# Kernel tuning notes

Measured on AMD Instinct MI355X. Metric: run time of the kernel, lower is better.

Reference implementation:

```python
import jax, jax.numpy as jnp
import numpy as np

T = 2048      # tokens
H = 1024      # hidden_size
HQ = 16       # num query heads
HK = 4        # num kv heads
D = 64        # head_dim
E = 8         # num experts
K = 2         # top_k
I = 2048      # expert intermediate size
EPS = 1e-5
THETA = 10000.0


def setup_inputs() -> dict:
    key = jax.random.key(0)
    ks = jax.random.split(key, 8)
    s = 0.02
    return {
        "hidden_states": jax.random.normal(ks[0], (T, H), jnp.float32),
        "positions": jnp.arange(T, dtype=jnp.int32),
        "qkv_w": jax.random.normal(ks[1], ((HQ + 2 * HK) * D, H), jnp.float32) * s,
        "o_w": jax.random.normal(ks[2], (H, HQ * D), jnp.float32) * s,
        "norm_in_w": jnp.ones((H,), jnp.float32),
        "norm_post_w": jnp.ones((H,), jnp.float32),
        "norm_next_w": jnp.ones((H,), jnp.float32),
        "gate_w": jax.random.normal(ks[3], (E, H), jnp.float32) * s,
        "w1": jax.random.normal(ks[4], (E, I, H), jnp.float32) * s,
        "w3": jax.random.normal(ks[5], (E, I, H), jnp.float32) * s,
        "w2": jax.random.normal(ks[6], (E, H, I), jnp.float32) * s,
    }


def rmsnorm(x, w):
    var = jnp.mean(x * x, axis=-1, keepdims=True)
    return x * jax.lax.rsqrt(var + EPS) * w


def rope_neox(x, positions):
    # x: [T, nH, D]; rotate-half (neox) style
    half = D // 2
    inv_freq = 1.0 / (THETA ** (jnp.arange(0, half, dtype=jnp.float32) * 2.0 / D))
    ang = positions.astype(jnp.float32)[:, None] * inv_freq[None, :]      # [T, D/2]
    cos = jnp.cos(ang)[:, None, :]
    sin = jnp.sin(ang)[:, None, :]
    x1, x2 = x[..., :half], x[..., half:]
    return jnp.concatenate([x1 * cos - x2 * sin, x2 * cos + x1 * sin], axis=-1)


def reference(hidden_states, positions, qkv_w, o_w, norm_in_w, norm_post_w,
              norm_next_w, gate_w, w1, w3, w2):
    x = hidden_states                               # [T, H]
    residual = x
    h = rmsnorm(x, norm_in_w)                       # input_layernorm

    # ---- attention (GQA, causal, neox RoPE) ----
    qkv = h @ qkv_w.T                               # [T, (HQ+2HK)*D]
    q, k, v = jnp.split(qkv, [HQ * D, (HQ + HK) * D], axis=-1)
    q = rope_neox(q.reshape(T, HQ, D), positions)
    k = rope_neox(k.reshape(T, HK, D), positions)
    v = v.reshape(T, HK, D)
    rep = HQ // HK
    k = jnp.repeat(k, rep, axis=1)                  # [T, HQ, D]
    v = jnp.repeat(v, rep, axis=1)
    scale = D ** -0.5
    scores = jnp.einsum('qhd,khd->hqk', q, k) * scale   # [HQ, T, T]
    mask = jnp.tril(jnp.ones((T, T), dtype=bool))
    scores = jnp.where(mask[None], scores, -jnp.inf)
    probs = jax.nn.softmax(scores, axis=-1)
    attn = jnp.einsum('hqk,khd->qhd', probs, v).reshape(T, HQ * D)
    attn_out = attn @ o_w.T                         # [T, H]

    # fused allreduce(identity, world=1) + residual add + post_attention RMSNorm
    residual = residual + attn_out
    h = rmsnorm(residual, norm_post_w)

    # ---- MoE: gate, top-2, renormalize, SiLU-gated experts ----
    logits = h @ gate_w.T                           # [T, E]
    route = jax.nn.softmax(logits, axis=-1)
    topw, topi = jax.lax.top_k(route, K)            # [T, K]
    topw = topw / jnp.sum(topw, axis=-1, keepdims=True)   # renormalize
    # dense combine weights [T, E] (zero for unselected experts)
    wdense = jnp.sum(jax.nn.one_hot(topi, E, dtype=h.dtype) * topw[..., None], axis=1)
    h1 = jnp.einsum('td,eid->tei', h, w1)           # [T, E, I]
    h3 = jnp.einsum('td,eid->tei', h, w3)
    gated = jax.nn.silu(h1) * h3
    moe_out = jnp.einsum('tei,edi,te->td', gated, w2, wdense)   # [T, H]

    # fused allreduce(identity) + residual add + next layer norm
    residual = residual + moe_out
    h = rmsnorm(residual, norm_next_w)
    return h
```

## Files before the change

kernel.cpp:

```cpp
#include <hip/hip_runtime.h>
#include <hip/hip_bf16.h>
#include <math.h>

#define T_ 2048
#define H_ 1024
#define HQ_ 16
#define HK_ 4
#define D_ 64
#define NE_ 8
#define II_ 2048

typedef __attribute__((ext_vector_type(8))) short bf16x8;
typedef __attribute__((ext_vector_type(8))) unsigned short u16x8;
typedef __attribute__((ext_vector_type(4))) float f32x4;

__device__ __forceinline__ unsigned short f2bf(float f) {
  unsigned int u = __float_as_uint(f);
  return (unsigned short)((u + 0x7fffu + ((u >> 16) & 1u)) >> 16);
}
__device__ __forceinline__ float bf2f(unsigned short h) {
  return __uint_as_float((unsigned int)h << 16);
}

__global__ __launch_bounds__(256) void k_rmsnorm(const float* __restrict__ x, const float* __restrict__ w,
                                                 float* __restrict__ outf, unsigned short* __restrict__ outb) {
  int row = blockIdx.x;
  int tid = threadIdx.x;
  float4 v = ((const float4*)(x + (size_t)row * H_))[tid];
  float ss = v.x * v.x + v.y * v.y + v.z * v.z + v.w * v.w;
#pragma unroll
  for (int off = 32; off; off >>= 1) ss += __shfl_xor(ss, off, 64);
  __shared__ float red[4];
  int lane = tid & 63, wid = tid >> 6;
  if (lane == 0) red[wid] = ss;
  __syncthreads();
  float tot = red[0] + red[1] + red[2] + red[3];
  float inv = rsqrtf(tot * (1.0f / H_) + 1e-5f);
  float4 wv = ((const float4*)w)[tid];
  float4 o;
  o.x = v.x * inv * wv.x; o.y = v.y * inv * wv.y; o.z = v.z * inv * wv.z; o.w = v.w * inv * wv.w;
  ((float4*)(outf + (size_t)row * H_))[tid] = o;
  if (outb) {
    ushort4 b; b.x = f2bf(o.x); b.y = f2bf(o.y); b.z = f2bf(o.z); b.w = f2bf(o.w);
    ((ushort4*)(outb + (size_t)row * H_))[tid] = b;
  }
}

__global__ __launch_bounds__(256) void k_rmsnorm_split(const float* __restrict__ x, const float* __restrict__ w,
                                                       unsigned short* __restrict__ Aq) {
  int row = blockIdx.x;
  int tid = threadIdx.x;
  float4 v = ((const float4*)(x + (size_t)row * H_))[tid];
  float ss = v.x * v.x + v.y * v.y + v.z * v.z + v.w * v.w;
#pragma unroll
  for (int off = 32; off; off >>= 1) ss += __shfl_xor(ss, off, 64);
  __shared__ float red[4];
  int lane = tid & 63, wid = tid >> 6;
  if (lane == 0) red[wid] = ss;
  __syncthreads();
  float tot = red[0] + red[1] + red[2] + red[3];
  float inv = rsqrtf(tot * (1.0f / H_) + 1e-5f);
  float4 wv = ((const float4*)w)[tid];
  float4 o;
  o.x = v.x * inv * wv.x; o.y = v.y * inv * wv.y; o.z = v.z * inv * wv.z; o.w = v.w * inv * wv.w;
  ushort4 hi, lo;
  hi.x = f2bf(o.x); hi.y = f2bf(o.y); hi.z = f2bf(o.z); hi.w = f2bf(o.w);
  lo.x = f2bf(o.x - bf2f(hi.x)); lo.y = f2bf(o.y - bf2f(hi.y));
  lo.z = f2bf(o.z - bf2f(hi.z)); lo.w = f2bf(o.w - bf2f(hi.w));
  size_t base = (size_t)row * (3 * H_) + tid * 4;
  *(ushort4*)(Aq + base) = hi;
  *(ushort4*)(Aq + base + H_) = hi;
  *(ushort4*)(Aq + base + 2 * H_) = lo;
}

__global__ __launch_bounds__(256) void k_wsplit(const float* __restrict__ in, unsigned short* __restrict__ out,
                                                int K, int n8total) {
  int stride = gridDim.x * 256;
  int kc8 = K >> 3;
  for (int i = blockIdx.x * 256 + threadIdx.x; i < n8total; i += stride) {
    int n = i / kc8, kc = (i - n * kc8) * 8;
    const float4* p = (const float4*)(in + (size_t)n * K + kc);
    float4 a = p[0], b = p[1];
    u16x8 hi, lo;
    hi[0] = f2bf(a.x); hi[1] = f2bf(a.y); hi[2] = f2bf(a.z); hi[3] = f2bf(a.w);
    hi[4] = f2bf(b.x); hi[5] = f2bf(b.y); hi[6] = f2bf(b.z); hi[7] = f2bf(b.w);
    lo[0] = f2bf(a.x - bf2f(hi[0])); lo[1] = f2bf(a.y - bf2f(hi[1]));
    lo[2] = f2bf(a.z - bf2f(hi[2])); lo[3] = f2bf(a.w - bf2f(hi[3]));
    lo[4] = f2bf(b.x - bf2f(hi[4])); lo[5] = f2bf(b.y - bf2f(hi[5]));
    lo[6] = f2bf(b.z - bf2f(hi[6])); lo[7] = f2bf(b.w - bf2f(hi[7]));
    size_t ob = (size_t)n * 3 * K + kc;
    *(u16x8*)(out + ob) = hi;
    *(u16x8*)(out + ob + K) = lo;
    *(u16x8*)(out + ob + 2 * K) = hi;
  }
}

template <int ADD>
__global__ __launch_bounds__(256) void k_hgemm(const unsigned short* __restrict__ A, const unsigned short* __restrict__ B,
                                               float* __restrict__ C, const float* __restrict__ addsrc,
                                               int N, int K3) {
  int m0 = blockIdx.y * 128, n0 = blockIdx.x * 64;
  __shared__ unsigned short As[2][128 * 72];
  __shared__ unsigned short Bs[2][64 * 72];
  int tid = threadIdx.x, lane = tid & 63, wid = tid >> 6;
  int wr = wid >> 1, wc = wid & 1;
  int l15 = lane & 15, lg = lane >> 4;
  int arow = tid >> 3, akg = (tid & 7) * 8;

  size_t aoff[4];
#pragma unroll
  for (int i = 0; i < 4; i++) aoff[i] = (size_t)(m0 + arow + 32 * i) * K3 + akg;
  size_t boff[2];
#pragma unroll
  for (int j = 0; j < 2; j++) boff[j] = (size_t)(n0 + arow + 32 * j) * K3 + akg;

  f32x4 acc[4][2];
  f32x4 z = {0.f, 0.f, 0.f, 0.f};
#pragma unroll
  for (int a = 0; a < 4; a++)
#pragma unroll
    for (int b = 0; b < 2; b++) acc[a][b] = z;

  uint4 pa[4], pb[2];
#pragma unroll
  for (int i = 0; i < 4; i++) pa[i] = *(const uint4*)(A + aoff[i]);
#pragma unroll
  for (int j = 0; j < 2; j++) pb[j] = *(const uint4*)(B + boff[j]);
#pragma unroll
  for (int i = 0; i < 4; i++) *(uint4*)&As[0][(arow + 32 * i) * 72 + akg] = pa[i];
#pragma unroll
  for (int j = 0; j < 2; j++) *(uint4*)&Bs[0][(arow + 32 * j) * 72 + akg] = pb[j];
  __syncthreads();
  int cur = 0;
  int nt = K3 / 64;
  for (int t = 0; t < nt; ++t) {
    if (t < nt - 1) {
      int kn = (t + 1) * 64;
#pragma unroll
      for (int i = 0; i < 4; i++) pa[i] = *(const uint4*)(A + aoff[i] + kn);
#pragma unroll
      for (int j = 0; j < 2; j++) pb[j] = *(const uint4*)(B + boff[j] + kn);
    }
#pragma unroll
    for (int kk = 0; kk < 2; kk++) {
      bf16x8 af[4], bw[2];
#pragma unroll
      for (int fa = 0; fa < 4; fa++)
        af[fa] = *(const bf16x8*)&As[cur][(wr * 64 + fa * 16 + l15) * 72 + kk * 32 + lg * 8];
#pragma unroll
      for (int fb = 0; fb < 2; fb++)
        bw[fb] = *(const bf16x8*)&Bs[cur][(wc * 32 + fb * 16 + l15) * 72 + kk * 32 + lg * 8];
#pragma unroll
      for (int fa = 0; fa < 4; fa++)
#pragma unroll
        for (int fb = 0; fb < 2; fb++)
          acc[fa][fb] = __builtin_amdgcn_mfma_f32_16x16x32_bf16(af[fa], bw[fb], acc[fa][fb], 0, 0, 0);
    }
    if (t < nt - 1) {
#pragma unroll
      for (int i = 0; i < 4; i++) *(uint4*)&As[cur ^ 1][(arow + 32 * i) * 72 + akg] = pa[i];
#pragma unroll
      for (int j = 0; j < 2; j++) *(uint4*)&Bs[cur ^ 1][(arow + 32 * j) * 72 + akg] = pb[j];
    }
    __syncthreads();
    cur ^= 1;
  }
#pragma unroll
  for (int fa = 0; fa < 4; fa++)
#pragma unroll
    for (int r = 0; r < 4; r++) {
      int row = m0 + wr * 64 + fa * 16 + lg * 4 + r;
#pragma unroll
      for (int fb = 0; fb < 2; fb++) {
        int col = n0 + wc * 32 + fb * 16 + l15;
        float v = acc[fa][fb][r];
        if (ADD) v += addsrc[(size_t)row * N + col];
        C[(size_t)row * N + col] = v;
      }
    }
}

__global__ __launch_bounds__(256) void k_rope_table(const int* __restrict__ pos, float* __restrict__ ct,
                                                    float* __restrict__ st) {
  int idx = blockIdx.x * 256 + threadIdx.x;
  int t = idx >> 5, i = idx & 31;
  float p = (float)pow(10000.0, (double)i / 32.0);
  float freq = 1.0f / p;
  float ang = (float)pos[t] * freq;
  ct[idx] = cosf(ang);
  st[idx] = sinf(ang);
}

__global__ __launch_bounds__(256) void k_rope_prep(const float* __restrict__ qkv, const float* __restrict__ ct,
                                                   const float* __restrict__ st, unsigned short* __restrict__ Qhi,
                                                   unsigned short* __restrict__ Qlo, unsigned short* __restrict__ Khi,
                                                   unsigned short* __restrict__ Klo) {
  int t = blockIdx.x, tid = threadIdx.x;
  const float* row = qkv + (size_t)t * 1536;
#pragma unroll 2
  for (int it = tid; it < 512; it += 256) {
    int h = it >> 5, i = it & 31;
    float c = ct[t * 32 + i], s = st[t * 32 + i];
    float x1 = row[h * 64 + i], x2 = row[h * 64 + i + 32];
    float a = (x1 * c - x2 * s) * 0.125f;
    float b = (x2 * c + x1 * s) * 0.125f;
    size_t base = ((size_t)h * T_ + t) * 64 + i;
    unsigned short ah = f2bf(a), bh = f2bf(b);
    Qhi[base] = ah; Qhi[base + 32] = bh;
    Qlo[base] = f2bf(a - bf2f(ah));
    Qlo[base + 32] = f2bf(b - bf2f(bh));
  }
  if (tid < 128) {
    int h = tid >> 5, i = tid & 31;
    float c = ct[t * 32 + i], s = st[t * 32 + i];
    float x1 = row[1024 + h * 64 + i], x2 = row[1024 + h * 64 + i + 32];
    float a = x1 * c - x2 * s;
    float b = x2 * c + x1 * s;
    size_t base = ((size_t)h * T_ + t) * 64 + i;
    unsigned short ah = f2bf(a), bh = f2bf(b);
    Khi[base] = ah; Khi[base + 32] = bh;
    Klo[base] = f2bf(a - bf2f(ah));
    Klo[base + 32] = f2bf(b - bf2f(bh));
  }
}

__global__ __launch_bounds__(256) void k_vtrans(const float* __restrict__ qkv, unsigned short* __restrict__ Vthi,
                                                unsigned short* __restrict__ Vtlo) {
  int t0 = blockIdx.x * 64, h = blockIdx.y;
  __shared__ float tile[64][65];
  int tid = threadIdx.x;
  int c = tid & 63, w = tid >> 6;
  for (int r = w; r < 64; r += 4)
    tile[r][c] = qkv[(size_t)(t0 + r) * 1536 + 1280 + h * 64 + c];
  __syncthreads();
  for (int d = w; d < 64; d += 4) {
    float v = tile[c][d];
    unsigned short hi = f2bf(v);
    size_t idx = ((size_t)h * 64 + d) * T_ + t0 + c;
    Vthi[idx] = hi;
    Vtlo[idx] = f2bf(v - bf2f(hi));
  }
}

__global__ __launch_bounds__(256) void k_attn_mfma(const unsigned short* __restrict__ Qhi,
                                                   const unsigned short* __restrict__ Qlo,
                                                   const unsigned short* __restrict__ Khi,
                                                   const unsigned short* __restrict__ Klo,
                                                   const unsigned short* __restrict__ Vthi,
                                                   const unsigned short* __restrict__ Vtlo,
                                                   unsigned short* __restrict__ Ao) {
  int bid = blockIdx.x;
  int kk = bid >> 4;
  int head = bid & 15;
  int qidx = (kk < 16) ? (31 - kk) : (kk - 16);
  int qb = qidx * 64;
  int kvh = head >> 2;
  int tid = threadIdx.x, lane = tid & 63, w = tid >> 6;
  int l15 = lane & 15, lg = lane >> 4;

  __shared__ unsigned short KsH[64 * 72], KsL[64 * 72];
  __shared__ unsigned short VsH[64 * 72], VsL[64 * 72];
  __shared__ unsigned short PsH[64 * 72], PsL[64 * 72];

  bf16x8 qh[2], ql[2];
  {
    size_t qbase = ((size_t)head * T_ + qb + w * 16 + l15) * 64 + lg * 8;
    qh[0] = *(const bf16x8*)(Qhi + qbase);
    qh[1] = *(const bf16x8*)(Qhi + qbase + 32);
    ql[0] = *(const bf16x8*)(Qlo + qbase);
    ql[1] = *(const bf16x8*)(Qlo + qbase + 32);
  }
  f32x4 z = {0.f, 0.f, 0.f, 0.f};
  f32x4 Oa[4];
  float mrow[4], lrow[4];
#pragma unroll
  for (int r = 0; r < 4; r++) { mrow[r] = -1e30f; lrow[r] = 0.f; }
#pragma unroll
  for (int dg = 0; dg < 4; dg++) Oa[dg] = z;

  for (int jb = 0; jb <= qb; jb += 64) {
    __syncthreads();
    for (int c = tid; c < 512; c += 256) {
      int r = c >> 3, g = (c & 7) * 8;
      size_t kgl = ((size_t)kvh * T_ + jb + r) * 64 + g;
      size_t vgl = ((size_t)kvh * 64 + r) * T_ + jb + g;
      *(uint4*)&KsH[r * 72 + g] = *(const uint4*)(Khi + kgl);
      *(uint4*)&KsL[r * 72 + g] = *(const uint4*)(Klo + kgl);
      *(uint4*)&VsH[r * 72 + g] = *(const uint4*)(Vthi + vgl);
      *(uint4*)&VsL[r * 72 + g] = *(const uint4*)(Vtlo + vgl);
    }
    __syncthreads();

    f32x4 sc[4];
    sc[0] = z; sc[1] = z; sc[2] = z; sc[3] = z;
#pragma unroll
    for (int kg = 0; kg < 4; kg++) {
      int ba = (kg * 16 + l15) * 72 + lg * 8;
      bf16x8 bh0 = *(const bf16x8*)&KsH[ba];
      bf16x8 bh1 = *(const bf16x8*)&KsH[ba + 32];
      bf16x8 bl0 = *(const bf16x8*)&KsL[ba];
      bf16x8 bl1 = *(const bf16x8*)&KsL[ba + 32];
      sc[kg] = __builtin_amdgcn_mfma_f32_16x16x32_bf16(qh[0], bh0, sc[kg], 0, 0, 0);
      sc[kg] = __builtin_amdgcn_mfma_f32_16x16x32_bf16(qh[1], bh1, sc[kg], 0, 0, 0);
      sc[kg] = __builtin_amdgcn_mfma_f32_16x16x32_bf16(qh[0], bl0, sc[kg], 0, 0, 0);
      sc[kg] = __builtin_amdgcn_mfma_f32_16x16x32_bf16(qh[1], bl1, sc[kg], 0, 0, 0);
      sc[kg] = __builtin_amdgcn_mfma_f32_16x16x32_bf16(ql[0], bh0, sc[kg], 0, 0, 0);
      sc[kg] = __builtin_amdgcn_mfma_f32_16x16x32_bf16(ql[1], bh1, sc[kg], 0, 0, 0);
    }
    if (jb == qb) {
      int rb = w * 16 + lg * 4;
#pragma unroll
      for (int kg = 0; kg < 4; kg++) {
        int col = kg * 16 + l15;
#pragma unroll
        for (int r = 0; r < 4; r++)
          if (col > rb + r) sc[kg][r] = -1e30f;
      }
    }
#pragma unroll
    for (int r = 0; r < 4; r++) {
      float mt = fmaxf(fmaxf(sc[0][r], sc[1][r]), fmaxf(sc[2][r], sc[3][r]));
      mt = fmaxf(mt, __shfl_xor(mt, 1, 64));
      mt = fmaxf(mt, __shfl_xor(mt, 2, 64));
      mt = fmaxf(mt, __shfl_xor(mt, 4, 64));
      mt = fmaxf(mt, __shfl_xor(mt, 8, 64));
      float mnew = fmaxf(mrow[r], mt);
      float corr = __expf(mrow[r] - mnew);
      mrow[r] = mnew;
      float s = 0.f;
#pragma unroll
      for (int kg = 0; kg < 4; kg++) {
        float p = __expf(sc[kg][r] - mnew);
        sc[kg][r] = p;
        s += p;
      }
      s += __shfl_xor(s, 1, 64);
      s += __shfl_xor(s, 2, 64);
      s += __shfl_xor(s, 4, 64);
      s += __shfl_xor(s, 8, 64);
      lrow[r] = lrow[r] * corr + s;
#pragma unroll
      for (int dg = 0; dg < 4; dg++) Oa[dg][r] *= corr;
    }
    {
      int rb = w * 16 + lg * 4;
#pragma unroll
      for (int kg = 0; kg < 4; kg++) {
        int col = kg * 16 + l15;
#pragma unroll
        for (int r = 0; r < 4; r++) {
          float p = sc[kg][r];
          unsigned short ph = f2bf(p);
          PsH[(rb + r) * 72 + col] = ph;
          PsL[(rb + r) * 72 + col] = f2bf(p - bf2f(ph));
        }
      }
    }
    {
      int ab = (w * 16 + l15) * 72 + lg * 8;
      bf16x8 ph0 = *(const bf16x8*)&PsH[ab];
      bf16x8 ph1 = *(const bf16x8*)&PsH[ab + 32];
      bf16x8 pl0 = *(const bf16x8*)&PsL[ab];
      bf16x8 pl1 = *(const bf16x8*)&PsL[ab + 32];
#pragma unroll
      for (int dg = 0; dg < 4; dg++) {
        int vb = (dg * 16 + l15) * 72 + lg * 8;
        bf16x8 vh0 = *(const bf16x8*)&VsH[vb];
        bf16x8 vh1 = *(const bf16x8*)&VsH[vb + 32];
        bf16x8 vl0 = *(const bf16x8*)&VsL[vb];
        bf16x8 vl1 = *(const bf16x8*)&VsL[vb + 32];
        Oa[dg] = __builtin_amdgcn_mfma_f32_16x16x32_bf16(ph0, vh0, Oa[dg], 0, 0, 0);
        Oa[dg] = __builtin_amdgcn_mfma_f32_16x16x32_bf16(ph1, vh1, Oa[dg], 0, 0, 0);
        Oa[dg] = __builtin_amdgcn_mfma_f32_16x16x32_bf16(ph0, vl0, Oa[dg], 0, 0, 0);
        Oa[dg] = __builtin_amdgcn_mfma_f32_16x16x32_bf16(ph1, vl1, Oa[dg], 0, 0, 0);
        Oa[dg] = __builtin_amdgcn_mfma_f32_16x16x32_bf16(pl0, vh0, Oa[dg], 0, 0, 0);
        Oa[dg] = __builtin_amdgcn_mfma_f32_16x16x32_bf16(pl1, vh1, Oa[dg], 0, 0, 0);
      }
    }
  }
#pragma unroll
  for (int r = 0; r < 4; r++) {
    float inv = 1.0f / lrow[r];
    size_t rb2 = (size_t)(qb + w * 16 + lg * 4 + r) * 3072 + head * 64;
#pragma unroll
    for (int dg = 0; dg < 4; dg++) {
      float v = Oa[dg][r] * inv;
      unsigned short hi = f2bf(v);
      unsigned short lo = f2bf(v - bf2f(hi));
      Ao[rb2 + dg * 16 + l15] = hi;
      Ao[rb2 + 1024 + dg * 16 + l15] = hi;
      Ao[rb2 + 2048 + dg * 16 + l15] = lo;
    }
  }
}

__global__ __launch_bounds__(256) void k_router(const float* __restrict__ h2, const float* __restrict__ gw,
                                                int* __restrict__ topi, float* __restrict__ topw,
                                                int* __restrict__ counts) {
  int wid = threadIdx.x >> 6, lane = threadIdx.x & 63;
  int t = blockIdx.x * 4 + wid;
  const float* hr = h2 + (size_t)t * H_;
  float hv[16];
#pragma unroll
  for (int i = 0; i < 16; i++) hv[i] = hr[lane + 64 * i];
  float le[8];
#pragma unroll
  for (int e = 0; e < 8; e++) {
    const float* g = gw + (size_t)e * H_;
    float acc = 0.f;
#pragma unroll
    for (int i = 0; i < 16; i++) acc += hv[i] * g[lane + 64 * i];
#pragma unroll
    for (int off = 32; off; off >>= 1) acc += __shfl_xor(acc, off, 64);
    le[e] = acc;
  }
  if (lane == 0) {
    int i0 = 0;
#pragma unroll
    for (int e = 1; e < 8; e++)
      if (le[e] > le[i0]) i0 = e;
    int i1 = (i0 == 0) ? 1 : 0;
#pragma unroll
    for (int e = 0; e < 8; e++) {
      if (e == i0) continue;
      if (le[e] > le[i1]) i1 = e;
    }
    float w1r = expf(le[i1] - le[i0]);
    float denom = 1.0f + w1r;
    topi[t * 2 + 0] = i0;
    topi[t * 2 + 1] = i1;
    topw[t * 2 + 0] = 1.0f / denom;
    topw[t * 2 + 1] = w1r / denom;
    atomicAdd(&counts[i0], 1);
    atomicAdd(&counts[i1], 1);
  }
}

__global__ void k_scan(const int* __restrict__ counts, int* __restrict__ offsets) {
  if (threadIdx.x == 0 && blockIdx.x == 0) {
    int off = 0;
    for (int e = 0; e < NE_; e++) { offsets[e] = off; off += counts[e]; }
  }
}

__global__ __launch_bounds__(256) void k_build(const int* __restrict__ topi, const float* __restrict__ topw,
                                               const int* __restrict__ offsets, int* __restrict__ counts2,
                                               int* __restrict__ pairs_ts, float* __restrict__ pairs_w) {
  int t = blockIdx.x * 256 + threadIdx.x;
#pragma unroll
  for (int s = 0; s < 2; s++) {
    int e = topi[t * 2 + s];
    int slot = atomicAdd(&counts2[e], 1);
    int p = offsets[e] + slot;
    pairs_ts[p] = t * 2 + s;
    pairs_w[p] = topw[t * 2 + s];
  }
}

__global__ __launch_bounds__(256) void k_conv(const float* __restrict__ in, unsigned short* __restrict__ out, int n8) {
  int stride = gridDim.x * 256;
  for (int i = blockIdx.x * 256 + threadIdx.x; i < n8; i += stride) {
    const float4* p = (const float4*)in + (size_t)i * 2;
    float4 a = p[0], b = p[1];
    u16x8 t;
    t[0] = f2bf(a.x); t[1] = f2bf(a.y); t[2] = f2bf(a.z); t[3] = f2bf(a.w);
    t[4] = f2bf(b.x); t[5] = f2bf(b.y); t[6] = f2bf(b.z); t[7] = f2bf(b.w);
    *((u16x8*)out + i) = t;
  }
}

__global__ __launch_bounds__(256) void k_moe_up(const unsigned short* __restrict__ h2b, const unsigned short* __restrict__ W1b,
                                                const unsigned short* __restrict__ W3b, const int* __restrict__ pairs_ts,
                                                const int* __restrict__ offsets, const int* __restrict__ counts,
                                                unsigned short* __restrict__ G) {
  int e = blockIdx.z;
  int ne = counts[e];
  int row0 = blockIdx.y * 128;
  if (row0 >= ne) return;
  int col0 = blockIdx.x * 64;
  int pbase = offsets[e];
  __shared__ unsigned short As[2][128 * 72];
  __shared__ unsigned short B1s[2][64 * 72];
  __shared__ unsigned short B2s[2][64 * 72];
  int tid = threadIdx.x, lane = tid & 63, wid = tid >> 6;
  int wr = wid >> 1, wc = wid & 1;
  int l15 = lane & 15, lg = lane >> 4;
  int arow = tid >> 3, akg = (tid & 7) * 8;

  int aoff[4];
#pragma unroll
  for (int i = 0; i < 4; i++) {
    int grow = row0 + arow + 32 * i;
    int tok = (grow < ne) ? (pairs_ts[pbase + grow] >> 1) : 0;
    aoff[i] = tok * H_ + akg;
  }
  size_t bbase = ((size_t)e * II_ + col0 + arow) * H_ + akg;

  f32x4 acc1[4][2], acc2[4][2];
  f32x4 z = {0.f, 0.f, 0.f, 0.f};
#pragma unroll
  for (int a = 0; a < 4; a++)
#pragma unroll
    for (int b = 0; b < 2; b++) { acc1[a][b] = z; acc2[a][b] = z; }

  uint4 pa[4], pb1[2], pb2[2];
#pragma unroll
  for (int i = 0; i < 4; i++) pa[i] = *(const uint4*)(h2b + aoff[i]);
#pragma unroll
  for (int j = 0; j < 2; j++) {
    pb1[j] = *(const uint4*)(W1b + bbase + (size_t)j * 32 * H_);
    pb2[j] = *(const uint4*)(W3b + bbase + (size_t)j * 32 * H_);
  }
#pragma unroll
  for (int i = 0; i < 4; i++) *(uint4*)&As[0][(arow + 32 * i) * 72 + akg] = pa[i];
#pragma unroll
  for (int j = 0; j < 2; j++) {
    *(uint4*)&B1s[0][(arow + 32 * j) * 72 + akg] = pb1[j];
    *(uint4*)&B2s[0][(arow + 32 * j) * 72 + akg] = pb2[j];
  }
  __syncthreads();
  int cur = 0;
  for (int t = 0; t < H_ / 64; ++t) {
    if (t < H_ / 64 - 1) {
      int kn = (t + 1) * 64;
#pragma unroll
      for (int i = 0; i < 4; i++) pa[i] = *(const uint4*)(h2b + aoff[i] + kn);
#pragma unroll
      for (int j = 0; j < 2; j++) {
        pb1[j] = *(const uint4*)(W1b + bbase + (size_t)j * 32 * H_ + kn);
        pb2[j] = *(const uint4*)(W3b + bbase + (size_t)j * 32 * H_ + kn);
      }
    }
#pragma unroll
    for (int kk = 0; kk < 2; kk++) {
      bf16x8 af[4], b1f[2], b2f[2];
#pragma unroll
      for (int fa = 0; fa < 4; fa++)
        af[fa] = *(const bf16x8*)&As[cur][(wr * 64 + fa * 16 + l15) * 72 + kk * 32 + lg * 8];
#pragma unroll
      for (int fb = 0; fb < 2; fb++) {
        b1f[fb] = *(const bf16x8*)&B1s[cur][(wc * 32 + fb * 16 + l15) * 72 + kk * 32 + lg * 8];
        b2f[fb] = *(const bf16x8*)&B2s[cur][(wc * 32 + fb * 16 + l15) * 72 + kk * 32 + lg * 8];
      }
#pragma unroll
      for (int fa = 0; fa < 4; fa++)
#pragma unroll
        for (int fb = 0; fb < 2; fb++) {
          acc1[fa][fb] = __builtin_amdgcn_mfma_f32_16x16x32_bf16(af[fa], b1f[fb], acc1[fa][fb], 0, 0, 0);
          acc2[fa][fb] = __builtin_amdgcn_mfma_f32_16x16x32_bf16(af[fa], b2f[fb], acc2[fa][fb], 0, 0, 0);
        }
    }
    if (t < H_ / 64 - 1) {
#pragma unroll
      for (int i = 0; i < 4; i++) *(uint4*)&As[cur ^ 1][(arow + 32 * i) * 72 + akg] = pa[i];
#pragma unroll
      for (int j = 0; j < 2; j++) {
        *(uint4*)&B1s[cur ^ 1][(arow + 32 * j) * 72 + akg] = pb1[j];
        *(uint4*)&B2s[cur ^ 1][(arow + 32 * j) * 72 + akg] = pb2[j];
      }
    }
    __syncthreads();
    cur ^= 1;
  }
#pragma unroll
  for (int fa = 0; fa < 4; fa++)
#pragma unroll
    for (int r = 0; r < 4; r++) {
      int prow = row0 + wr * 64 + fa * 16 + lg * 4 + r;
      if (prow < ne) {
#pragma unroll
        for (int fb = 0; fb < 2; fb++) {
          int icol = col0 + wc * 32 + fb * 16 + l15;
          float h1 = acc1[fa][fb][r], h3 = acc2[fa][fb][r];
          float g = h1 / (1.0f + __expf(-h1)) * h3;
          G[(size_t)(pbase + prow) * II_ + icol] = f2bf(g);
        }
      }
    }
}

__global__ __launch_bounds__(256) void k_moe_down(const unsigned short* __restrict__ G, const unsigned short* __restrict__ W2b,
                                                  const int* __restrict__ pairs_ts, const float* __restrict__ pairs_w,
                                                  const int* __restrict__ offsets, const int* __restrict__ counts,
                                                  float* __restrict__ Pbuf) {
  int e = blockIdx.z;
  int ne = counts[e];
  int row0 = blockIdx.y * 128;
  if (row0 >= ne) return;
  int col0 = blockIdx.x * 64;
  int pbase = offsets[e];
  __shared__ unsigned short As[2][128 * 72];
  __shared__ unsigned short Bs[2][64 * 72];
  int tid = threadIdx.x, lane = tid & 63, wid = tid >> 6;
  int wr = wid >> 1, wc = wid & 1;
  int l15 = lane & 15, lg = lane >> 4;
  int arow = tid >> 3, akg = (tid & 7) * 8;

  int aoff[4];
#pragma unroll
  for (int i = 0; i < 4; i++) {
    int grow = row0 + arow + 32 * i;
    int p = pbase + ((grow < ne) ? grow : 0);
    aoff[i] = p * II_ + akg;
  }
  size_t bbase = ((size_t)e * H_ + col0 + arow) * II_ + akg;

  f32x4 acc[4][2];
  f32x4 z = {0.f, 0.f, 0.f, 0.f};
#pragma unroll
  for (int a = 0; a < 4; a++)
#pragma unroll
    for (int b = 0; b < 2; b++) acc[a][b] = z;

  uint4 pa[4], pb[2];
#pragma unroll
  for (int i = 0; i < 4; i++) pa[i] = *(const uint4*)(G + aoff[i]);
#pragma unroll
  for (int j = 0; j < 2; j++) pb[j] = *(const uint4*)(W2b + bbase + (size_t)j * 32 * II_);
#pragma unroll
  for (int i = 0; i < 4; i++) *(uint4*)&As[0][(arow + 32 * i) * 72 + akg] = pa[i];
#pragma unroll
  for (int j = 0; j < 2; j++) *(uint4*)&Bs[0][(arow + 32 * j) * 72 + akg] = pb[j];
  __syncthreads();
  int cur = 0;
  for (int t = 0; t < II_ / 64; ++t) {
    if (t < II_ / 64 - 1) {
      int kn = (t + 1) * 64;
#pragma unroll
      for (int i = 0; i < 4; i++) pa[i] = *(const uint4*)(G + aoff[i] + kn);
#pragma unroll
      for (int j = 0; j < 2; j++) pb[j] = *(const uint4*)(W2b + bbase + (size_t)j * 32 * II_ + kn);
    }
#pragma unroll
    for (int kk = 0; kk < 2; kk++) {
      bf16x8 af[4], bw[2];
#pragma unroll
      for (int fa = 0; fa < 4; fa++)
        af[fa] = *(const bf16x8*)&As[cur][(wr * 64 + fa * 16 + l15) * 72 + kk * 32 + lg * 8];
#pragma unroll
      for (int fb = 0; fb < 2; fb++)
        bw[fb] = *(const bf16x8*)&Bs[cur][(wc * 32 + fb * 16 + l15) * 72 + kk * 32 + lg * 8];
#pragma unroll
      for (int fa = 0; fa < 4; fa++)
#pragma unroll
        for (int fb = 0; fb < 2; fb++)
          acc[fa][fb] = __builtin_amdgcn_mfma_f32_16x16x32_bf16(af[fa], bw[fb], acc[fa][fb], 0, 0, 0);
    }
    if (t < II_ / 64 - 1) {
#pragma unroll
      for (int i = 0; i < 4; i++) *(uint4*)&As[cur ^ 1][(arow + 32 * i) * 72 + akg] = pa[i];
#pragma unroll
      for (int j = 0; j < 2; j++) *(uint4*)&Bs[cur ^ 1][(arow + 32 * j) * 72 + akg] = pb[j];
    }
    __syncthreads();
    cur ^= 1;
  }
#pragma unroll
  for (int fa = 0; fa < 4; fa++)
#pragma unroll
    for (int r = 0; r < 4; r++) {
      int prow = row0 + wr * 64 + fa * 16 + lg * 4 + r;
      if (prow < ne) {
        int p = pbase + prow;
        int ts = pairs_ts[p];
        float wgt = pairs_w[p];
#pragma unroll
        for (int fb = 0; fb < 2; fb++) {
          int col = col0 + wc * 32 + fb * 16 + l15;
          Pbuf[(size_t)ts * H_ + col] = wgt * acc[fa][fb][r];
        }
      }
    }
}

__global__ __launch_bounds__(256) void k_final(const float* __restrict__ resid, const float* __restrict__ Pbuf,
                                               const float* __restrict__ w, float* __restrict__ out) {
  int row = blockIdx.x;
  int tid = threadIdx.x;
  float4 a = ((const float4*)(resid + (size_t)row * H_))[tid];
  float4 p0 = ((const float4*)(Pbuf + (size_t)(2 * row) * H_))[tid];
  float4 p1 = ((const float4*)(Pbuf + (size_t)(2 * row + 1) * H_))[tid];
  float4 v;
  v.x = a.x + p0.x + p1.x; v.y = a.y + p0.y + p1.y; v.z = a.z + p0.z + p1.z; v.w = a.w + p0.w + p1.w;
  float ss = v.x * v.x + v.y * v.y + v.z * v.z + v.w * v.w;
#pragma unroll
  for (int off = 32; off; off >>= 1) ss += __shfl_xor(ss, off, 64);
  __shared__ float red[4];
  int lane = tid & 63, wid = tid >> 6;
  if (lane == 0) red[wid] = ss;
  __syncthreads();
  float tot = red[0] + red[1] + red[2] + red[3];
  float inv = rsqrtf(tot * (1.0f / H_) + 1e-5f);
  float4 wv = ((const float4*)w)[tid];
  float4 o;
  o.x = v.x * inv * wv.x; o.y = v.y * inv * wv.y; o.z = v.z * inv * wv.z; o.w = v.w * inv * wv.w;
  ((float4*)(out + (size_t)row * H_))[tid] = o;
}

extern "C" void kernel_launch(void* const* d_in, const int* in_sizes, int n_in,
                              void* d_out, int out_size, void* d_ws, size_t ws_size,
                              hipStream_t stream) {
  const float* x = (const float*)d_in[0];
  const int* pos = (const int*)d_in[1];
  const float* qkv_w = (const float*)d_in[2];
  const float* o_w = (const float*)d_in[3];
  const float* nin_w = (const float*)d_in[4];
  const float* npost_w = (const float*)d_in[5];
  const float* nnext_w = (const float*)d_in[6];
  const float* gate_w = (const float*)d_in[7];
  const float* w1 = (const float*)d_in[8];
  const float* w3 = (const float*)d_in[9];
  const float* w2 = (const float*)d_in[10];
  float* out = (float*)d_out;

  float* resid = (float*)d_ws;
  float* h2 = resid + (size_t)T_ * H_;
  float* Pbuf = h2 + (size_t)T_ * H_;
  float* topw = Pbuf + (size_t)2 * T_ * H_;
  float* pairsw = topw + T_ * 2;
  unsigned short* h2b = (unsigned short*)(pairsw + 4096);
  unsigned short* G = h2b + (size_t)T_ * H_;
  int* topi = (int*)(G + (size_t)2 * T_ * II_);
  int* ctrl = topi + T_ * 2;
  int* counts = ctrl;
  int* counts2 = ctrl + 8;
  int* offsets = ctrl + 16;
  int* pairs_ts = ctrl + 24;
  char* trans = (char*)(pairs_ts + 4096);
  trans = (char*)(((uintptr_t)trans + 255) & ~(uintptr_t)255);

  unsigned short* Aq = (unsigned short*)trans;
  unsigned short* Bq = Aq + (size_t)T_ * 3072;
  unsigned short* Bo = Bq + (size_t)1536 * 3072;
  unsigned short* Ao = Bo + (size_t)1024 * 3072;
  float* qkvb = (float*)(Ao + (size_t)T_ * 3072);
  float* ct = qkvb + (size_t)T_ * 1536;
  float* st = ct + (size_t)T_ * 32;
  unsigned short* uu = (unsigned short*)(st + (size_t)T_ * 32);
  unsigned short* Qhi = uu;  uu += (size_t)HQ_ * T_ * D_;
  unsigned short* Qlo = uu;  uu += (size_t)HQ_ * T_ * D_;
  unsigned short* Khi = uu;  uu += (size_t)HK_ * T_ * D_;
  unsigned short* Klo = uu;  uu += (size_t)HK_ * T_ * D_;
  unsigned short* Vthi = uu; uu += (size_t)HK_ * D_ * T_;
  unsigned short* Vtlo = uu; uu += (size_t)HK_ * D_ * T_;

  unsigned short* W1b = (unsigned short*)trans;
  unsigned short* W3b = W1b + (size_t)NE_ * II_ * H_;
  unsigned short* W2b = W3b + (size_t)NE_ * II_ * H_;

  const int WCNT8 = (NE_ * II_ * H_) / 8;

  hipMemsetAsync(ctrl, 0, 64, stream);
  k_rmsnorm_split<<<T_, 256, 0, stream>>>(x, nin_w, Aq);
  k_wsplit<<<2048, 256, 0, stream>>>(qkv_w, Bq, H_, 1536 * H_ / 8);
  k_wsplit<<<2048, 256, 0, stream>>>(o_w, Bo, HQ_ * D_, H_ * HQ_ * D_ / 8);
  k_hgemm<0><<<dim3(1536 / 64, T_ / 128), 256, 0, stream>>>(Aq, Bq, qkvb, nullptr, 1536, 3 * H_);
  k_rope_table<<<T_ * 32 / 256, 256, 0, stream>>>(pos, ct, st);
  k_rope_prep<<<T_, 256, 0, stream>>>(qkvb, ct, st, Qhi, Qlo, Khi, Klo);
  k_vtrans<<<dim3(T_ / 64, HK_), 256, 0, stream>>>(qkvb, Vthi, Vtlo);
  k_attn_mfma<<<dim3(512), 256, 0, stream>>>(Qhi, Qlo, Khi, Klo, Vthi, Vtlo, Ao);
  k_hgemm<1><<<dim3(H_ / 64, T_ / 128), 256, 0, stream>>>(Ao, Bo, resid, x, H_, 3 * HQ_ * D_);
  k_rmsnorm<<<T_, 256, 0, stream>>>(resid, npost_w, h2, h2b);
  k_router<<<T_ / 4, 256, 0, stream>>>(h2, gate_w, topi, topw, counts);
  k_scan<<<1, 64, 0, stream>>>(counts, offsets);
  k_build<<<T_ / 256, 256, 0, stream>>>(topi, topw, offsets, counts2, pairs_ts, pairsw);
  k_conv<<<2048, 256, 0, stream>>>(w1, W1b, WCNT8);
  k_conv<<<2048, 256, 0, stream>>>(w3, W3b, WCNT8);
  k_conv<<<2048, 256, 0, stream>>>(w2, W2b, WCNT8);
  k_moe_up<<<dim3(II_ / 64, T_ / 128, NE_), 256, 0, stream>>>(h2b, W1b, W3b, pairs_ts, offsets, counts, G);
  k_moe_down<<<dim3(H_ / 64, T_ / 128, NE_), 256, 0, stream>>>(G, W2b, pairs_ts, pairsw, offsets, counts, Pbuf);
  k_final<<<T_, 256, 0, stream>>>(resid, Pbuf, nnext_w, out);
}
```

Baseline: 551.1 us.

## Use direct global-to-LDS loads in GEMM and MoE kernels with K-tile 32

Replaces the register-staged global loads and LDS stores in the dense GEMM, MoE up and MoE down kernels with global_load_lds direct-to-LDS transfers. The K tile shrinks from 64 to 32 and the padded 72-wide LDS rows become unpadded 32-wide rows. This removes VGPR staging and the explicit ds_write traffic, which frees registers. In exchange it doubles the number of barriers per K, has no padding so LDS bank conflicts are possible on fragment reads, and gives less compute per tile to hide load latency.

```diff
diff --git a/kernel.cpp b/kernel.cpp
--- a/kernel.cpp
+++ b/kernel.cpp
@@ -13,6 +13,10 @@
 typedef __attribute__((ext_vector_type(8))) short bf16x8;
 typedef __attribute__((ext_vector_type(8))) unsigned short u16x8;
 typedef __attribute__((ext_vector_type(4))) float f32x4;
+
+#define GLOAD16(g, l)                                                                   \
+  __builtin_amdgcn_global_load_lds((const __attribute__((address_space(1))) unsigned int*)(g), \
+                                   (__attribute__((address_space(3))) unsigned int*)(l), 16, 0, 0)
 
 __device__ __forceinline__ unsigned short f2bf(float f) {
   unsigned int u = __float_as_uint(f);
@@ -100,19 +104,16 @@
                                                float* __restrict__ C, const float* __restrict__ addsrc,
                                                int N, int K3) {
   int m0 = blockIdx.y * 128, n0 = blockIdx.x * 64;
-  __shared__ unsigned short As[2][128 * 72];
-  __shared__ unsigned short Bs[2][64 * 72];
-  int tid = threadIdx.x, lane = tid & 63, wid = tid >> 6;
-  int wr = wid >> 1, wc = wid & 1;
+  __shared__ unsigned short As[2][128 * 32];
+  __shared__ unsigned short Bs[2][64 * 32];
+  int tid = threadIdx.x, lane = tid & 63, w = tid >> 6;
+  int wr = w >> 1, wc = w & 1;
   int l15 = lane & 15, lg = lane >> 4;
-  int arow = tid >> 3, akg = (tid & 7) * 8;
-
-  size_t aoff[4];
-#pragma unroll
-  for (int i = 0; i < 4; i++) aoff[i] = (size_t)(m0 + arow + 32 * i) * K3 + akg;
-  size_t boff[2];
-#pragma unroll
-  for (int j = 0; j < 2; j++) boff[j] = (size_t)(n0 + arow + 32 * j) * K3 + akg;
+  int srow = lane >> 2, schunk = lane & 3;
+
+  const unsigned short* ga0 = A + (size_t)(m0 + w * 32 + srow) * K3 + schunk * 8;
+  const unsigned short* ga1 = A + (size_t)(m0 + w * 32 + 16 + srow) * K3 + schunk * 8;
+  const unsigned short* gb = B + (size_t)(n0 + w * 16 + srow) * K3 + schunk * 8;
 
   f32x4 acc[4][2];
   f32x4 z = {0.f, 0.f, 0.f, 0.f};
@@ -121,49 +122,33 @@
 #pragma unroll
     for (int b = 0; b < 2; b++) acc[a][b] = z;
 
-  uint4 pa[4], pb[2];
-#pragma unroll
-  for (int i = 0; i < 4; i++) pa[i] = *(const uint4*)(A + aoff[i]);
-#pragma unroll
-  for (int j = 0; j < 2; j++) pb[j] = *(const uint4*)(B + boff[j]);
-#pragma unroll
-  for (int i = 0; i < 4; i++) *(uint4*)&As[0][(arow + 32 * i) * 72 + akg] = pa[i];
-#pragma unroll
-  for (int j = 0; j < 2; j++) *(uint4*)&Bs[0][(arow + 32 * j) * 72 + akg] = pb[j];
+  GLOAD16(ga0, &As[0][(w * 32) * 32]);
+  GLOAD16(ga1, &As[0][(w * 32 + 16) * 32]);
+  GLOAD16(gb, &Bs[0][(w * 16) * 32]);
   __syncthreads();
-  int cur = 0;
-  int nt = K3 / 64;
+
+  int nt = K3 / 32;
   for (int t = 0; t < nt; ++t) {
-    if (t < nt - 1) {
-      int kn = (t + 1) * 64;
-#pragma unroll
-      for (int i = 0; i < 4; i++) pa[i] = *(const uint4*)(A + aoff[i] + kn);
-#pragma unroll
-      for (int j = 0; j < 2; j++) pb[j] = *(const uint4*)(B + boff[j] + kn);
-    }
-#pragma unroll
-    for (int kk = 0; kk < 2; kk++) {
-      bf16x8 af[4], bw[2];
-#pragma unroll
-      for (int fa = 0; fa < 4; fa++)
-        af[fa] = *(const bf16x8*)&As[cur][(wr * 64 + fa * 16 + l15) * 72 + kk * 32 + lg * 8];
+    int cur = t & 1;
+    if (t + 1 < nt) {
+      int ko = (t + 1) * 32;
+      GLOAD16(ga0 + ko, &As[cur ^ 1][(w * 32) * 32]);
+      GLOAD16(ga1 + ko, &As[cur ^ 1][(w * 32 + 16) * 32]);
+      GLOAD16(gb + ko, &Bs[cur ^ 1][(w * 16) * 32]);
+    }
+    bf16x8 af[4], bw2[2];
+#pragma unroll
+    for (int fa = 0; fa < 4; fa++)
+      af[fa] = *(const bf16x8*)&As[cur][(wr * 64 + fa * 16 + l15) * 32 + lg * 8];
+#pragma unroll
+    for (int fb = 0; fb < 2; fb++)
+      bw2[fb] = *(const bf16x8*)&Bs[cur][(wc * 32 + fb * 16 + l15) * 32 + lg * 8];
+#pragma unroll
+    for (int fa = 0; fa < 4; fa++)
 #pragma unroll
       for (int fb = 0; fb < 2; fb++)
-        bw[fb] = *(const bf16x8*)&Bs[cur][(wc * 32 + fb * 16 + l15) * 72 + kk * 32 + lg * 8];
-#pragma unroll
-      for (int fa = 0; fa < 4; fa++)
-#pragma unroll
-        for (int fb = 0; fb < 2; fb++)
-          acc[fa][fb] = __builtin_amdgcn_mfma_f32_16x16x32_bf16(af[fa], bw[fb], acc[fa][fb], 0, 0, 0);
-    }
-    if (t < nt - 1) {
-#pragma unroll
-      for (int i = 0; i < 4; i++) *(uint4*)&As[cur ^ 1][(arow + 32 * i) * 72 + akg] = pa[i];
-#pragma unroll
-      for (int j = 0; j < 2; j++) *(uint4*)&Bs[cur ^ 1][(arow + 32 * j) * 72 + akg] = pb[j];
-    }
+        acc[fa][fb] = __builtin_amdgcn_mfma_f32_16x16x32_bf16(af[fa], bw2[fb], acc[fa][fb], 0, 0, 0);
     __syncthreads();
-    cur ^= 1;
   }
 #pragma unroll
   for (int fa = 0; fa < 4; fa++)
@@ -479,22 +464,21 @@
   if (row0 >= ne) return;
   int col0 = blockIdx.x * 64;
   int pbase = offsets[e];
-  __shared__ unsigned short As[2][128 * 72];
-  __shared__ unsigned short B1s[2][64 * 72];
-  __shared__ unsigned short B2s[2][64 * 72];
-  int tid = threadIdx.x, lane = tid & 63, wid = tid >> 6;
-  int wr = wid >> 1, wc = wid & 1;
+  __shared__ unsigned short As[2][128 * 32];
+  __shared__ unsigned short B1s[2][64 * 32];
+  __shared__ unsigned short B2s[2][64 * 32];
+  int tid = threadIdx.x, lane = tid & 63, w = tid >> 6;
+  int wr = w >> 1, wc = w & 1;
   int l15 = lane & 15, lg = lane >> 4;
-  int arow = tid >> 3, akg = (tid & 7) * 8;
-
-  int aoff[4];
-#pragma unroll
-  for (int i = 0; i < 4; i++) {
-    int grow = row0 + arow + 32 * i;
-    int tok = (grow < ne) ? (pairs_ts[pbase + grow] >> 1) : 0;
-    aoff[i] = tok * H_ + akg;
-  }
-  size_t bbase = ((size_t)e * II_ + col0 + arow) * H_ + akg;
+  int srow = lane >> 2, schunk = lane & 3;
+
+  int gr0 = row0 + w * 32 + srow, gr1 = gr0 + 16;
+  int tok0 = (gr0 < ne) ? (pairs_ts[pbase + gr0] >> 1) : 0;
+  int tok1 = (gr1 < ne) ? (pairs_ts[pbase + gr1] >> 1) : 0;
+  const unsigned short* ga0 = h2b + (size_t)tok0 * H_ + schunk * 8;
+  const unsigned short* ga1 = h2b + (size_t)tok1 * H_ + schunk * 8;
+  const unsigned short* gb1 = W1b + ((size_t)e * II_ + col0 + w * 16 + srow) * H_ + schunk * 8;
+  const unsigned short* gb3 = W3b + ((size_t)e * II_ + col0 + w * 16 + srow) * H_ + schunk * 8;
 
   f32x4 acc1[4][2], acc2[4][2];
   f32x4 z = {0.f, 0.f, 0.f, 0.f};
@@ -503,64 +487,38 @@
 #pragma unroll
     for (int b = 0; b < 2; b++) { acc1[a][b] = z; acc2[a][b] = z; }
 
-  uint4 pa[4], pb1[2], pb2[2];
-#pragma unroll
-  for (int i = 0; i < 4; i++) pa[i] = *(const uint4*)(h2b + aoff[i]);
-#pragma unroll
-  for (int j = 0; j < 2; j++) {
-    pb1[j] = *(const uint4*)(W1b + bbase + (size_t)j * 32 * H_);
-    pb2[j] = *(const uint4*)(W3b + bbase + (size_t)j * 32 * H_);
-  }
-#pragma unroll
-  for (int i = 0; i < 4; i++) *(uint4*)&As[0][(arow + 32 * i) * 72 + akg] = pa[i];
-#pragma unroll
-  for (int j = 0; j < 2; j++) {
-    *(uint4*)&B1s[0][(arow + 32 * j) * 72 + akg] = pb1[j];
-    *(uint4*)&B2s[0][(arow + 32 * j) * 72 + akg] = pb2[j];
-  }
+  GLOAD16(ga0, &As[0][(w * 32) * 32]);
+  GLOAD16(ga1, &As[0][(w * 32 + 16) * 32]);
+  GLOAD16(gb1, &B1s[0][(w * 16) * 32]);
+  GLOAD16(gb3, &B2s[0][(w * 16) * 32]);
   __syncthreads();
-  int cur = 0;
-  for (int t = 0; t < H_ / 64; ++t) {
-    if (t < H_ / 64 - 1) {
-      int kn = (t + 1) * 64;
-#pragma unroll
-      for (int i = 0; i < 4; i++) pa[i] = *(const uint4*)(h2b + aoff[i] + kn);
-#pragma unroll
-      for (int j = 0; j < 2; j++) {
-        pb1[j] = *(const uint4*)(W1b + bbase + (size_t)j * 32 * H_ + kn);
-        pb2[j] = *(const uint4*)(W3b + bbase + (size_t)j * 32 * H_ + kn);
+
+  for (int t = 0; t < H_ / 32; ++t) {
+    int cur = t & 1;
+    if (t + 1 < H_ / 32) {
+      int ko = (t + 1) * 32;
+      GLOAD16(ga0 + ko, &As[cur ^ 1][(w * 32) * 32]);
+      GLOAD16(ga1 + ko, &As[cur ^ 1][(w * 32 + 16) * 32]);
+      GLOAD16(gb1 + ko, &B1s[cur ^ 1][(w * 16) * 32]);
+      GLOAD16(gb3 + ko, &B2s[cur ^ 1][(w * 16) * 32]);
+    }
+    bf16x8 af[4], b1f[2], b2f[2];
+#pragma unroll
+    for (int fa = 0; fa < 4; fa++)
+      af[fa] = *(const bf16x8*)&As[cur][(wr * 64 + fa * 16 + l15) * 32 + lg * 8];
+#pragma unroll
+    for (int fb = 0; fb < 2; fb++) {
+      b1f[fb] = *(const bf16x8*)&B1s[cur][(wc * 32 + fb * 16 + l15) * 32 + lg * 8];
+      b2f[fb] = *(const bf16x8*)&B2s[cur][(wc * 32 + fb * 16 + l15) * 32 + lg * 8];
+    }
+#pragma unroll
+    for (int fa = 0; fa < 4; fa++)
+#pragma unroll
+      for (int fb = 0; fb < 2; fb++) {
+        acc1[fa][fb] = __builtin_amdgcn_mfma_f32_16x16x32_bf16(af[fa], b1f[fb], acc1[fa][fb], 0, 0, 0);
+        acc2[fa][fb] = __builtin_amdgcn_mfma_f32_16x16x32_bf16(af[fa], b2f[fb], acc2[fa][fb], 0, 0, 0);
       }
-    }
-#pragma unroll
-    for (int kk = 0; kk < 2; kk++) {
-      bf16x8 af[4], b1f[2], b2f[2];
-#pragma unroll
-      for (int fa = 0; fa < 4; fa++)
-        af[fa] = *(const bf16x8*)&As[cur][(wr * 64 + fa * 16 + l15) * 72 + kk * 32 + lg * 8];
-#pragma unroll
-      for (int fb = 0; fb < 2; fb++) {
-        b1f[fb] = *(const bf16x8*)&B1s[cur][(wc * 32 + fb * 16 + l15) * 72 + kk * 32 + lg * 8];
-        b2f[fb] = *(const bf16x8*)&B2s[cur][(wc * 32 + fb * 16 + l15) * 72 + kk * 32 + lg * 8];
-      }
-#pragma unroll
-      for (int fa = 0; fa < 4; fa++)
-#pragma unroll
-        for (int fb = 0; fb < 2; fb++) {
-          acc1[fa][fb] = __builtin_amdgcn_mfma_f32_16x16x32_bf16(af[fa], b1f[fb], acc1[fa][fb], 0, 0, 0);
-          acc2[fa][fb] = __builtin_amdgcn_mfma_f32_16x16x32_bf16(af[fa], b2f[fb], acc2[fa][fb], 0, 0, 0);
-        }
-    }
-    if (t < H_ / 64 - 1) {
-#pragma unroll
-      for (int i = 0; i < 4; i++) *(uint4*)&As[cur ^ 1][(arow + 32 * i) * 72 + akg] = pa[i];
-#pragma unroll
-      for (int j = 0; j < 2; j++) {
-        *(uint4*)&B1s[cur ^ 1][(arow + 32 * j) * 72 + akg] = pb1[j];
-        *(uint4*)&B2s[cur ^ 1][(arow + 32 * j) * 72 + akg] = pb2[j];
-      }
-    }
     __syncthreads();
-    cur ^= 1;
   }
 #pragma unroll
   for (int fa = 0; fa < 4; fa++)
@@ -589,21 +547,19 @@
   if (row0 >= ne) return;
   int col0 = blockIdx.x * 64;
   int pbase = offsets[e];
-  __shared__ unsigned short As[2][128 * 72];
-  __shared__ unsigned short Bs[2][64 * 72];
-  int tid = threadIdx.x, lane = tid & 63, wid = tid >> 6;
-  int wr = wid >> 1, wc = wid & 1;
+  __shared__ unsigned short As[2][128 * 32];
+  __shared__ unsigned short Bs[2][64 * 32];
+  int tid = threadIdx.x, lane = tid & 63, w = tid >> 6;
+  int wr = w >> 1, wc = w & 1;
   int l15 = lane & 15, lg = lane >> 4;
-  int arow = tid >> 3, akg = (tid & 7) * 8;
-
-  int aoff[4];
-#pragma unroll
-  for (int i = 0; i < 4; i++) {
-    int grow = row0 + arow + 32 * i;
-    int p = pbase + ((grow < ne) ? grow : 0);
-    aoff[i] = p * II_ + akg;
-  }
-  size_t bbase = ((size_t)e * H_ + col0 + arow) * II_ + akg;
+  int srow = lane >> 2, schunk = lane & 3;
+
+  int gr0 = row0 + w * 32 + srow, gr1 = gr0 + 16;
+  int p0 = pbase + ((gr0 < ne) ? gr0 : 0);
+  int p1 = pbase + ((gr1 < ne) ? gr1 : 0);
+  const unsigned short* ga0 = G + (size_t)p0 * II_ + schunk * 8;
+  const unsigned short* ga1 = G + (size_t)p1 * II_ + schunk * 8;
+  const unsigned short* gb = W2b + ((size_t)e * H_ + col0 + w * 16 + srow) * II_ + schunk * 8;
 
   f32x4 acc[4][2];
   f32x4 z = {0.f, 0.f, 0.f, 0.f};
@@ -612,48 +568,32 @@
 #pragma unroll
     for (int b = 0; b < 2; b++) acc[a][b] = z;
 
-  uint4 pa[4], pb[2];
-#pragma unroll
-  for (int i = 0; i < 4; i++) pa[i] = *(const uint4*)(G + aoff[i]);
-#pragma unroll
-  for (int j = 0; j < 2; j++) pb[j] = *(const uint4*)(W2b + bbase + (size_t)j * 32 * II_);
-#pragma unroll
-  for (int i = 0; i < 4; i++) *(uint4*)&As[0][(arow + 32 * i) * 72 + akg] = pa[i];
-#pragma unroll
-  for (int j = 0; j < 2; j++) *(uint4*)&Bs[0][(arow + 32 * j) * 72 + akg] = pb[j];
+  GLOAD16(ga0, &As[0][(w * 32) * 32]);
+  GLOAD16(ga1, &As[0][(w * 32 + 16) * 32]);
+  GLOAD16(gb, &Bs[0][(w * 16) * 32]);
   __syncthreads();
-  int cur = 0;
-  for (int t = 0; t < II_ / 64; ++t) {
-    if (t < II_ / 64 - 1) {
-      int kn = (t + 1) * 64;
-#pragma unroll
-      for (int i = 0; i < 4; i++) pa[i] = *(const uint4*)(G + aoff[i] + kn);
-#pragma unroll
-      for (int j = 0; j < 2; j++) pb[j] = *(const uint4*)(W2b + bbase + (size_t)j * 32 * II_ + kn);
-    }
-#pragma unroll
-    for (int kk = 0; kk < 2; kk++) {
-      bf16x8 af[4], bw[2];
-#pragma unroll
-      for (int fa = 0; fa < 4; fa++)
-        af[fa] = *(const bf16x8*)&As[cur][(wr * 64 + fa * 16 + l15) * 72 + kk * 32 + lg * 8];
+
+  for (int t = 0; t < II_ / 32; ++t) {
+    int cur = t & 1;
+    if (t + 1 < II_ / 32) {
+      int ko = (t + 1) * 32;
+      GLOAD16(ga0 + ko, &As[cur ^ 1][(w * 32) * 32]);
+      GLOAD16(ga1 + ko, &As[cur ^ 1][(w * 32 + 16) * 32]);
+      GLOAD16(gb + ko, &Bs[cur ^ 1][(w * 16) * 32]);
+    }
+    bf16x8 af[4], bw2[2];
+#pragma unroll
+    for (int fa = 0; fa < 4; fa++)
+      af[fa] = *(const bf16x8*)&As[cur][(wr * 64 + fa * 16 + l15) * 32 + lg * 8];
+#pragma unroll
+    for (int fb = 0; fb < 2; fb++)
+      bw2[fb] = *(const bf16x8*)&Bs[cur][(wc * 32 + fb * 16 + l15) * 32 + lg * 8];
+#pragma unroll
+    for (int fa = 0; fa < 4; fa++)
 #pragma unroll
       for (int fb = 0; fb < 2; fb++)
-        bw[fb] = *(const bf16x8*)&Bs[cur][(wc * 32 + fb * 16 + l15) * 72 + kk * 32 + lg * 8];
-#pragma unroll
-      for (int fa = 0; fa < 4; fa++)
-#pragma unroll
-        for (int fb = 0; fb < 2; fb++)
-          acc[fa][fb] = __builtin_amdgcn_mfma_f32_16x16x32_bf16(af[fa], bw[fb], acc[fa][fb], 0, 0, 0);
-    }
-    if (t < II_ / 64 - 1) {
-#pragma unroll
-      for (int i = 0; i < 4; i++) *(uint4*)&As[cur ^ 1][(arow + 32 * i) * 72 + akg] = pa[i];
-#pragma unroll
-      for (int j = 0; j < 2; j++) *(uint4*)&Bs[cur ^ 1][(arow + 32 * j) * 72 + akg] = pb[j];
-    }
+        acc[fa][fb] = __builtin_amdgcn_mfma_f32_16x16x32_bf16(af[fa], bw2[fb], acc[fa][fb], 0, 0, 0);
     __syncthreads();
-    cur ^= 1;
   }
 #pragma unroll
   for (int fa = 0; fa < 4; fa++)
```

New measurement: 489.1 us. -11.2%, faster.
